# Kernel optimization log

Measured on AMD Instinct MI355X. Metric: run time of the kernel, lower is better.

Reference implementation:

```python
import jax, jax.numpy as jnp
import numpy as np

B, N, M = 8, 2048, 2048
DQ = DK = DV = H = O = 1024

def setup_inputs() -> dict:
    key = jax.random.key(0)
    ks = jax.random.split(key, 10)
    input_query = jax.random.normal(ks[0], (B, N, DQ), dtype=jnp.float32)
    input_key = jax.random.normal(ks[1], (B, M, DK), dtype=jnp.float32)
    input_value = jax.random.normal(ks[2], (B, M, DV), dtype=jnp.float32)
    seq_lens = jax.random.randint(ks[3], (B,), 1, M + 1)
    seq_lens = seq_lens.at[0].set(M)  # original asserts max(seq_lens) == M
    s = 1.0 / np.sqrt(DQ)
    Wq = jax.random.normal(ks[4], (DQ, H), dtype=jnp.float32) * s
    bq = jnp.zeros((H,), dtype=jnp.float32)
    Wk = jax.random.normal(ks[5], (DK, H), dtype=jnp.float32) * s
    bk = jnp.zeros((H,), dtype=jnp.float32)
    Wv = jax.random.normal(ks[6], (DV, O), dtype=jnp.float32) * s
    bv = jnp.zeros((O,), dtype=jnp.float32)
    return {"input_query": input_query, "input_key": input_key, "input_value": input_value,
            "seq_lens": seq_lens, "Wq": Wq, "bq": bq, "Wk": Wk, "bk": bk, "Wv": Wv, "bv": bv}


def reference(input_query, input_key, input_value, seq_lens, Wq, bq, Wk, bk, Wv, bv):
    hidden_dim = Wq.shape[1]
    lq = input_query @ Wq + bq          # (B, N, H)
    lk = input_key @ Wk + bk            # (B, M, H)
    lv = input_value @ Wv + bv          # (B, M, O)
    scores = jnp.einsum('bnh,bmh->bnm', lq, lk) / jnp.sqrt(jnp.float32(hidden_dim))
    # additive mask: 0 for valid positions, finfo.min for padded (as in original)
    valid = (jnp.arange(scores.shape[-1]) < seq_lens[:, None])[:, None, :]  # (B,1,M)
    add_mask = jnp.where(valid, 0.0, jnp.finfo(scores.dtype).min)
    scores = scores + add_mask
    probs = jax.nn.softmax(scores, axis=-1)
    out = jnp.einsum('bnm,bmo->bno', probs, lv)  # dropout is identity in eval
    return out
```

## Files before the change

kernel.cpp:

```cpp
#include <hip/hip_runtime.h>
#include <hip/hip_bf16.h>

typedef unsigned short u16;
typedef __attribute__((ext_vector_type(8))) short bfrag;
typedef __attribute__((ext_vector_type(4))) float f32x4;
typedef __attribute__((ext_vector_type(8))) unsigned short us8;
typedef __attribute__((ext_vector_type(4))) unsigned short us4;

__device__ __forceinline__ u16 f2bf(float f) {
  union { float f; unsigned int u; } x; x.f = f;
  unsigned int r = x.u + 0x7fffu + ((x.u >> 16) & 1u);
  return (u16)(r >> 16);
}
__device__ __forceinline__ float bf2f(u16 u) {
  union { unsigned int u; float f; } x; x.u = ((unsigned int)u) << 16;
  return x.f;
}

__device__ __forceinline__ void gld16(const void* g, void* l) {
  __builtin_amdgcn_global_load_lds((const __attribute__((address_space(1))) void*)g,
                                   (__attribute__((address_space(3))) void*)l, 16, 0, 0);
}

__global__ __launch_bounds__(256) void transpose_w(const float* __restrict__ W0,
                                                   const float* __restrict__ W1,
                                                   const float* __restrict__ W2,
                                                   u16* __restrict__ T0,
                                                   u16* __restrict__ T1,
                                                   u16* __restrict__ T2) {
  const float* W = (blockIdx.z == 0) ? W0 : ((blockIdx.z == 1) ? W1 : W2);
  u16* T = (blockIdx.z == 0) ? T0 : ((blockIdx.z == 1) ? T1 : T2);
  __shared__ u16 tile[64][72];
  const int t = threadIdx.x;
  const int rr = t >> 4;
  const int cc = (t & 15) * 4;
  const int kbase = blockIdx.y * 64, nbase = blockIdx.x * 64;
#pragma unroll
  for (int j = 0; j < 4; ++j) {
    int kl = rr + j * 16;
    float4 v = *(const float4*)(W + (size_t)(kbase + kl) * 1024 + nbase + cc);
    tile[kl][cc + 0] = f2bf(v.x);
    tile[kl][cc + 1] = f2bf(v.y);
    tile[kl][cc + 2] = f2bf(v.z);
    tile[kl][cc + 3] = f2bf(v.w);
  }
  __syncthreads();
#pragma unroll
  for (int j = 0; j < 4; ++j) {
    int nl = rr + j * 16;
    us4 o;
    o[0] = tile[cc + 0][nl];
    o[1] = tile[cc + 1][nl];
    o[2] = tile[cc + 2][nl];
    o[3] = tile[cc + 3][nl];
    *(us4*)(T + (size_t)(nbase + nl) * 1024 + kbase + cc) = o;
  }
}

__global__ __launch_bounds__(256) void cvt_bf16(const float* __restrict__ src,
                                                u16* __restrict__ dst, int n8) {
  int i = blockIdx.x * blockDim.x + threadIdx.x;
  const int stride = gridDim.x * blockDim.x;
  for (; i < n8; i += stride) {
    const float4* p = (const float4*)(src + (size_t)i * 8);
    float4 v0 = p[0], v1 = p[1];
    us8 o;
    o[0] = f2bf(v0.x); o[1] = f2bf(v0.y); o[2] = f2bf(v0.z); o[3] = f2bf(v0.w);
    o[4] = f2bf(v1.x); o[5] = f2bf(v1.y); o[6] = f2bf(v1.z); o[7] = f2bf(v1.w);
    *(us8*)(dst + (size_t)i * 8) = o;
  }
}

template <int OUT>
__global__ __launch_bounds__(512, 2) void gemm256(const u16* __restrict__ gA,
                                                  const u16* __restrict__ gB,
                                                  const float* __restrict__ bias,
                                                  void* __restrict__ outp,
                                                  int K, int ldc,
                                                  size_t aStride, size_t bStride,
                                                  size_t cStride,
                                                  const int* __restrict__ seq) {
  __shared__ u16 lds[65536];
  const int tid = threadIdx.x;

  const int id = blockIdx.x + gridDim.x * (blockIdx.y + gridDim.y * blockIdx.z);
  int bx, by, bz;
  if constexpr (OUT == 0 || OUT == 2) {
    bx = (id >> 3) & 3; by = (id & 7) + 8 * (id >> 5); bz = 0;
  } else if constexpr (OUT == 1) {
    bx = (id >> 3) & 7; by = id & 7; bz = id >> 6;
  } else {
    bx = (id >> 3) & 3; by = id & 7; bz = id >> 5;
  }

  const u16* A = gA + (size_t)bz * aStride;
  const u16* B = gB + (size_t)bz * bStride;
  const int brow = by * 256, bcol = bx * 256;

  const int NT = K >> 6;
  int NTe = NT;
  if constexpr (OUT == 1) {
    if (bcol >= seq[bz]) return;
  }
  if constexpr (OUT == 3) {
    const int len = seq[bz];
    const int nt2 = (len + 63) >> 6;
    NTe = nt2 < NT ? nt2 : NT;
  }

  const int wv = tid >> 6, l = tid & 63;
  const int wm = wv >> 2, wn = wv & 3;
  const int fr = l & 15, fq = l >> 4;
  const int g0 = (fq ^ (fr & 7)) * 8;
  const int g1 = ((4 + fq) ^ (fr & 7)) * 8;

  const int srow = tid >> 3;
  const int sg = (tid & 7) ^ (srow & 7);
  const u16* aS = A + (size_t)(brow + srow) * K + sg * 8;
  const u16* bS = B + (size_t)(bcol + srow) * K + sg * 8;
  u16* const dA = lds + wv * 512;
  u16* const dB = lds + 32768 + wv * 512;

  f32x4 acc[8][4] = {};

  auto stA = [&](int tile, int c, int buf) {
    gld16(aS + (size_t)tile * 64 + (size_t)c * 64 * K, dA + buf * 16384 + c * 4096);
  };
  auto stB = [&](int tile, int c, int buf) {
    gld16(bS + (size_t)tile * 64 + (size_t)c * 64 * K, dB + buf * 16384 + c * 4096);
  };

#pragma unroll
  for (int c = 0; c < 4; ++c) stA(0, c, 0);
#pragma unroll
  for (int c = 0; c < 4; ++c) stB(0, c, 0);
  if (NTe > 1) {
    stA(1, 0, 1); stA(1, 2, 1);
    stB(1, 0, 1); stB(1, 1, 1); stB(1, 2, 1); stB(1, 3, 1);
  }

  for (int t = 0; t < NTe; ++t) {
    const int cur = t & 1;
    const u16* At = lds + cur * 16384;
    const u16* Bt = lds + 32768 + cur * 16384;

    if (t + 1 < NTe) asm volatile("s_waitcnt vmcnt(6)" ::: "memory");
    else             asm volatile("s_waitcnt vmcnt(0)" ::: "memory");
    __builtin_amdgcn_s_barrier();

    bfrag a[4][2], b[2][2][2];

#pragma unroll
    for (int m = 0; m < 4; ++m) {
      const u16* p = At + (wm * 128 + m * 16 + fr) * 64;
      a[m][0] = *(const bfrag*)(p + g0);
      a[m][1] = *(const bfrag*)(p + g1);
    }
#pragma unroll
    for (int n = 0; n < 2; ++n) {
      const u16* p = Bt + (wn * 64 + n * 16 + fr) * 64;
      b[0][n][0] = *(const bfrag*)(p + g0);
      b[0][n][1] = *(const bfrag*)(p + g1);
    }
    if (t + 1 < NTe) { stA(t + 1, 1, cur ^ 1); stA(t + 1, 3, cur ^ 1); }
    __builtin_amdgcn_s_barrier();
    asm volatile("s_waitcnt lgkmcnt(0)" ::: "memory");
    __builtin_amdgcn_sched_barrier(0);
    __builtin_amdgcn_s_setprio(1);
#pragma unroll
    for (int n = 0; n < 2; ++n)
#pragma unroll
      for (int m = 0; m < 4; ++m) {
        acc[m][n] = __builtin_amdgcn_mfma_f32_16x16x32_bf16(a[m][0], b[0][n][0], acc[m][n], 0, 0, 0);
        acc[m][n] = __builtin_amdgcn_mfma_f32_16x16x32_bf16(a[m][1], b[0][n][1], acc[m][n], 0, 0, 0);
      }
    __builtin_amdgcn_s_setprio(0);
    __builtin_amdgcn_s_barrier();

#pragma unroll
    for (int n = 0; n < 2; ++n) {
      const u16* p = Bt + (wn * 64 + 32 + n * 16 + fr) * 64;
      b[1][n][0] = *(const bfrag*)(p + g0);
      b[1][n][1] = *(const bfrag*)(p + g1);
    }
    if (t + 2 < NTe) { stA(t + 2, 0, cur); stA(t + 2, 2, cur); }
    __builtin_amdgcn_s_barrier();
    asm volatile("s_waitcnt lgkmcnt(0)" ::: "memory");
    __builtin_amdgcn_sched_barrier(0);
    __builtin_amdgcn_s_setprio(1);
#pragma unroll
    for (int n = 0; n < 2; ++n)
#pragma unroll
      for (int m = 0; m < 4; ++m) {
        acc[m][2 + n] = __builtin_amdgcn_mfma_f32_16x16x32_bf16(a[m][0], b[1][n][0], acc[m][2 + n], 0, 0, 0);
        acc[m][2 + n] = __builtin_amdgcn_mfma_f32_16x16x32_bf16(a[m][1], b[1][n][1], acc[m][2 + n], 0, 0, 0);
      }
    __builtin_amdgcn_s_setprio(0);
    __builtin_amdgcn_s_barrier();

#pragma unroll
    for (int m = 0; m < 4; ++m) {
      const u16* p = At + (wm * 128 + 64 + m * 16 + fr) * 64;
      a[m][0] = *(const bfrag*)(p + g0);
      a[m][1] = *(const bfrag*)(p + g1);
    }
    if (t + 2 < NTe) { stB(t + 2, 0, cur); stB(t + 2, 1, cur); }
    __builtin_amdgcn_s_barrier();
    asm volatile("s_waitcnt lgkmcnt(0)" ::: "memory");
    __builtin_amdgcn_sched_barrier(0);
    __builtin_amdgcn_s_setprio(1);
#pragma unroll
    for (int n = 0; n < 2; ++n)
#pragma unroll
      for (int m = 0; m < 4; ++m) {
        acc[4 + m][n] = __builtin_amdgcn_mfma_f32_16x16x32_bf16(a[m][0], b[0][n][0], acc[4 + m][n], 0, 0, 0);
        acc[4 + m][n] = __builtin_amdgcn_mfma_f32_16x16x32_bf16(a[m][1], b[0][n][1], acc[4 + m][n], 0, 0, 0);
      }
    __builtin_amdgcn_s_setprio(0);
    __builtin_amdgcn_s_barrier();

    if (t + 2 < NTe) { stB(t + 2, 2, cur); stB(t + 2, 3, cur); }
    __builtin_amdgcn_s_setprio(1);
#pragma unroll
    for (int n = 0; n < 2; ++n)
#pragma unroll
      for (int m = 0; m < 4; ++m) {
        acc[4 + m][2 + n] = __builtin_amdgcn_mfma_f32_16x16x32_bf16(a[m][0], b[1][n][0], acc[4 + m][2 + n], 0, 0, 0);
        acc[4 + m][2 + n] = __builtin_amdgcn_mfma_f32_16x16x32_bf16(a[m][1], b[1][n][1], acc[4 + m][2 + n], 0, 0, 0);
      }
    __builtin_amdgcn_s_setprio(0);
  }

#pragma unroll
  for (int mg = 0; mg < 8; ++mg) {
    const int r0 = brow + wm * 128 + mg * 16 + fq * 4;
#pragma unroll
    for (int n = 0; n < 4; ++n) {
      const int c = bcol + wn * 64 + n * 16 + fr;
      f32x4 vv = acc[mg][n];
      if constexpr (OUT == 0) {
        float bb = bias[c];
        u16* C = (u16*)outp;
#pragma unroll
        for (int j = 0; j < 4; ++j) C[(size_t)(r0 + j) * ldc + c] = f2bf(vv[j] + bb);
      } else if constexpr (OUT == 1) {
        u16* C = (u16*)outp + (size_t)bz * cStride;
#pragma unroll
        for (int j = 0; j < 4; ++j) C[(size_t)(r0 + j) * ldc + c] = f2bf(vv[j] * 0.03125f);
      } else if constexpr (OUT == 2) {
        float bb = bias[c];
        const int bz2 = r0 >> 11, mm = r0 & 2047;
        us4 o;
#pragma unroll
        for (int j = 0; j < 4; ++j) o[j] = f2bf(vv[j] + bb);
        *(us4*)((u16*)outp + ((size_t)bz2 * 1024 + c) * 2048 + mm) = o;
      } else {
        float* C = (float*)outp + (size_t)bz * cStride;
#pragma unroll
        for (int j = 0; j < 4; ++j) C[(size_t)(r0 + j) * ldc + c] = vv[j];
      }
    }
  }
}

__global__ __launch_bounds__(256) void softmax_mask(u16* __restrict__ probs,
                                                    const int* __restrict__ seq) {
  const int bid = blockIdx.x;
  const int b = bid >> 11, n = bid & 2047;
  const int len = seq[b];
  const int len64 = (len + 63) & ~63;
  u16* row = probs + ((size_t)b * 2048 + n) * 2048;
  const int t = threadIdx.x;
  const int w = t >> 6, l = t & 63;

  us8 sv = {};
  if (t * 8 < len) sv = *(const us8*)(row + t * 8);
  float vals[8];
  float vmax = -1e30f;
#pragma unroll
  for (int e = 0; e < 8; ++e) {
    int m = t * 8 + e;
    float x = bf2f(sv[e]);
    vals[e] = (m < len) ? x : -1e30f;
    vmax = fmaxf(vmax, vals[e]);
  }
#pragma unroll
  for (int o = 32; o > 0; o >>= 1) vmax = fmaxf(vmax, __shfl_xor(vmax, o, 64));
  __shared__ float sm[4], ss[4];
  if (l == 0) sm[w] = vmax;
  __syncthreads();
  vmax = fmaxf(fmaxf(sm[0], sm[1]), fmaxf(sm[2], sm[3]));

  float ev[8];
  float sum = 0.f;
#pragma unroll
  for (int e = 0; e < 8; ++e) {
    int m = t * 8 + e;
    float p = (m < len) ? __expf(vals[e] - vmax) : 0.f;
    ev[e] = p;
    sum += p;
  }
#pragma unroll
  for (int o = 32; o > 0; o >>= 1) sum += __shfl_xor(sum, o, 64);
  if (l == 0) ss[w] = sum;
  __syncthreads();
  sum = ss[0] + ss[1] + ss[2] + ss[3];
  float inv = 1.f / sum;
  if (t * 8 < len64) {
    us8 ov;
#pragma unroll
    for (int e = 0; e < 8; ++e) ov[e] = f2bf(ev[e] * inv);
    *(us8*)(row + t * 8) = ov;
  }
}

extern "C" void kernel_launch(void* const* d_in, const int* in_sizes, int n_in,
                              void* d_out, int out_size, void* d_ws, size_t ws_size,
                              hipStream_t stream) {
  const float* q   = (const float*)d_in[0];
  const float* k   = (const float*)d_in[1];
  const float* v   = (const float*)d_in[2];
  const int*   seq = (const int*)d_in[3];
  const float* Wq  = (const float*)d_in[4];
  const float* bq  = (const float*)d_in[5];
  const float* Wk  = (const float*)d_in[6];
  const float* bk  = (const float*)d_in[7];
  const float* Wv  = (const float*)d_in[8];
  const float* bv  = (const float*)d_in[9];
  float* out = (float*)d_out;

  u16* ws = (u16*)d_ws;
  u16* wtq = ws;
  u16* wtk = wtq + (size_t)1024 * 1024;
  u16* wtv = wtk + (size_t)1024 * 1024;
  u16* lq  = wtv + (size_t)1024 * 1024;
  u16* lk  = lq + (size_t)16384 * 1024;
  u16* lvt = lk + (size_t)16384 * 1024;
  u16* probs = lvt + (size_t)16384 * 1024;
  u16* cbuf = probs;

  const size_t S21 = (size_t)2048 * 1024;
  const size_t S22 = (size_t)2048 * 2048;

  transpose_w<<<dim3(16, 16, 3), 256, 0, stream>>>(Wq, Wk, Wv, wtq, wtk, wtv);

  cvt_bf16<<<dim3(2048), 256, 0, stream>>>(q, cbuf, 2097152);
  gemm256<0><<<dim3(4, 64, 1), 512, 0, stream>>>(cbuf, wtq, bq, lq, 1024, 1024, 0, 0, 0, nullptr);
  cvt_bf16<<<dim3(2048), 256, 0, stream>>>(k, cbuf, 2097152);
  gemm256<0><<<dim3(4, 64, 1), 512, 0, stream>>>(cbuf, wtk, bk, lk, 1024, 1024, 0, 0, 0, nullptr);
  cvt_bf16<<<dim3(2048), 256, 0, stream>>>(v, cbuf, 2097152);
  gemm256<2><<<dim3(4, 64, 1), 512, 0, stream>>>(cbuf, wtv, bv, lvt, 1024, 1024, 0, 0, 0, nullptr);

  gemm256<1><<<dim3(8, 8, 8), 512, 0, stream>>>(lq, lk, nullptr, probs, 1024, 2048, S21, S21, S22, seq);
  softmax_mask<<<dim3(16384), 256, 0, stream>>>(probs, seq);
  gemm256<3><<<dim3(4, 8, 8), 512, 0, stream>>>(probs, lvt, nullptr, out, 2048, 1024, S22, S21, S21, seq);
}
```

Baseline: 320.8 us.

## Replace 256-tile pipelined GEMM with simpler 128-tile GEMM fusing fp32-to-bf16 conversion

Replaces the hand-pipelined 256x256 double-buffered GEMM with a simpler 128x128 single-buffered GEMM using K-step 32 and 256 threads. The projection GEMMs now read fp32 activations directly and convert them to bf16 while storing into LDS, which removes the three separate cvt_bf16 kernels and their intermediate buffer traffic. The block-id swizzle for L2 locality is also changed. The cost is losing the overlap of global loads with MFMA work, since each K step now waits on a barrier before computing, and the smaller tiles give less data reuse.

Result: slower. 397.9 us (+24.0%).

```diff
diff --git a/kernel.cpp b/kernel.cpp
--- a/kernel.cpp
+++ b/kernel.cpp
@@ -57,22 +57,8 @@
   }
 }
 
-__global__ __launch_bounds__(256) void cvt_bf16(const float* __restrict__ src,
-                                                u16* __restrict__ dst, int n8) {
-  int i = blockIdx.x * blockDim.x + threadIdx.x;
-  const int stride = gridDim.x * blockDim.x;
-  for (; i < n8; i += stride) {
-    const float4* p = (const float4*)(src + (size_t)i * 8);
-    float4 v0 = p[0], v1 = p[1];
-    us8 o;
-    o[0] = f2bf(v0.x); o[1] = f2bf(v0.y); o[2] = f2bf(v0.z); o[3] = f2bf(v0.w);
-    o[4] = f2bf(v1.x); o[5] = f2bf(v1.y); o[6] = f2bf(v1.z); o[7] = f2bf(v1.w);
-    *(us8*)(dst + (size_t)i * 8) = o;
-  }
-}
-
 template <int OUT>
-__global__ __launch_bounds__(512, 2) void gemm256(const u16* __restrict__ gA,
+__global__ __launch_bounds__(256, 4) void gemm128(const void* __restrict__ gAv,
                                                   const u16* __restrict__ gB,
                                                   const float* __restrict__ bias,
                                                   void* __restrict__ outp,
@@ -80,164 +66,105 @@
                                                   size_t aStride, size_t bStride,
                                                   size_t cStride,
                                                   const int* __restrict__ seq) {
-  __shared__ u16 lds[65536];
+  constexpr bool AF32 = (OUT == 0 || OUT == 2);
+  __shared__ u16 Ab[4096];
+  __shared__ u16 Bb[4096];
   const int tid = threadIdx.x;
 
-  const int id = blockIdx.x + gridDim.x * (blockIdx.y + gridDim.y * blockIdx.z);
   int bx, by, bz;
-  if constexpr (OUT == 0 || OUT == 2) {
-    bx = (id >> 3) & 3; by = (id & 7) + 8 * (id >> 5); bz = 0;
-  } else if constexpr (OUT == 1) {
-    bx = (id >> 3) & 7; by = id & 7; bz = id >> 6;
+  if constexpr (AF32) {
+    const int gx = gridDim.x, gy = gridDim.y;
+    const int nwg = gx * gy;
+    int id = blockIdx.x + gx * blockIdx.y;
+    id = (id & 7) * (nwg >> 3) + (id >> 3);
+    bx = id % gx; by = id / gx; bz = 0;
   } else {
-    bx = (id >> 3) & 3; by = id & 7; bz = id >> 5;
-  }
-
-  const u16* A = gA + (size_t)bz * aStride;
+    bx = blockIdx.x; by = blockIdx.y; bz = blockIdx.z;
+  }
+
   const u16* B = gB + (size_t)bz * bStride;
-  const int brow = by * 256, bcol = bx * 256;
-
-  const int NT = K >> 6;
+  const int brow = by * 128, bcol = bx * 128;
+
+  const int NT = K >> 5;
   int NTe = NT;
   if constexpr (OUT == 1) {
     if (bcol >= seq[bz]) return;
   }
   if constexpr (OUT == 3) {
     const int len = seq[bz];
-    const int nt2 = (len + 63) >> 6;
+    const int nt2 = (len + 31) >> 5;
     NTe = nt2 < NT ? nt2 : NT;
   }
 
   const int wv = tid >> 6, l = tid & 63;
-  const int wm = wv >> 2, wn = wv & 3;
+  const int wm = wv >> 1, wn = wv & 1;
   const int fr = l & 15, fq = l >> 4;
-  const int g0 = (fq ^ (fr & 7)) * 8;
-  const int g1 = ((4 + fq) ^ (fr & 7)) * 8;
-
-  const int srow = tid >> 3;
-  const int sg = (tid & 7) ^ (srow & 7);
-  const u16* aS = A + (size_t)(brow + srow) * K + sg * 8;
-  const u16* bS = B + (size_t)(bcol + srow) * K + sg * 8;
-  u16* const dA = lds + wv * 512;
-  u16* const dB = lds + 32768 + wv * 512;
-
-  f32x4 acc[8][4] = {};
-
-  auto stA = [&](int tile, int c, int buf) {
-    gld16(aS + (size_t)tile * 64 + (size_t)c * 64 * K, dA + buf * 16384 + c * 4096);
-  };
-  auto stB = [&](int tile, int c, int buf) {
-    gld16(bS + (size_t)tile * 64 + (size_t)c * 64 * K, dB + buf * 16384 + c * 4096);
-  };
-
-#pragma unroll
-  for (int c = 0; c < 4; ++c) stA(0, c, 0);
-#pragma unroll
-  for (int c = 0; c < 4; ++c) stB(0, c, 0);
-  if (NTe > 1) {
-    stA(1, 0, 1); stA(1, 2, 1);
-    stB(1, 0, 1); stB(1, 1, 1); stB(1, 2, 1); stB(1, 3, 1);
-  }
+  const int goff = (fq ^ ((fr >> 1) & 3)) * 8;
+
+  const int sr = tid >> 2;
+  const int sg = (tid & 3) ^ ((tid >> 3) & 3);
+  const int phys8 = (tid & 3) * 8;
+
+  const float* Af = (const float*)gAv;
+  const u16* Ab16 = (const u16*)gAv + (size_t)bz * aStride;
+  const u16* bS = B + (size_t)(bcol + sr) * K + sg * 8;
+  u16* const dA = Ab + wv * 512;
+  u16* const dB = Bb + wv * 512;
+
+  f32x4 acc[4][4] = {};
 
   for (int t = 0; t < NTe; ++t) {
-    const int cur = t & 1;
-    const u16* At = lds + cur * 16384;
-    const u16* Bt = lds + 32768 + cur * 16384;
-
-    if (t + 1 < NTe) asm volatile("s_waitcnt vmcnt(6)" ::: "memory");
-    else             asm volatile("s_waitcnt vmcnt(0)" ::: "memory");
-    __builtin_amdgcn_s_barrier();
-
-    bfrag a[4][2], b[2][2][2];
-
-#pragma unroll
-    for (int m = 0; m < 4; ++m) {
-      const u16* p = At + (wm * 128 + m * 16 + fr) * 64;
-      a[m][0] = *(const bfrag*)(p + g0);
-      a[m][1] = *(const bfrag*)(p + g1);
+    const int k0 = t << 5;
+    if constexpr (AF32) {
+      float4 va[2][2];
+#pragma unroll
+      for (int u = 0; u < 2; ++u) {
+        const float* ap = Af + (size_t)(brow + u * 64 + sr) * K + k0 + sg * 8;
+        va[u][0] = *(const float4*)ap;
+        va[u][1] = *(const float4*)(ap + 4);
+      }
+      gld16(bS + k0, dB);
+      gld16(bS + k0 + (size_t)64 * K, dB + 2048);
+#pragma unroll
+      for (int u = 0; u < 2; ++u) {
+        us8 pk;
+        pk[0] = f2bf(va[u][0].x); pk[1] = f2bf(va[u][0].y);
+        pk[2] = f2bf(va[u][0].z); pk[3] = f2bf(va[u][0].w);
+        pk[4] = f2bf(va[u][1].x); pk[5] = f2bf(va[u][1].y);
+        pk[6] = f2bf(va[u][1].z); pk[7] = f2bf(va[u][1].w);
+        *(us8*)(Ab + (u * 64 + sr) * 32 + phys8) = pk;
+      }
+    } else {
+      const u16* aS = Ab16 + (size_t)(brow + sr) * K + k0 + sg * 8;
+      gld16(aS, dA);
+      gld16(aS + (size_t)64 * K, dA + 2048);
+      gld16(bS + k0, dB);
+      gld16(bS + k0 + (size_t)64 * K, dB + 2048);
     }
-#pragma unroll
-    for (int n = 0; n < 2; ++n) {
-      const u16* p = Bt + (wn * 64 + n * 16 + fr) * 64;
-      b[0][n][0] = *(const bfrag*)(p + g0);
-      b[0][n][1] = *(const bfrag*)(p + g1);
-    }
-    if (t + 1 < NTe) { stA(t + 1, 1, cur ^ 1); stA(t + 1, 3, cur ^ 1); }
-    __builtin_amdgcn_s_barrier();
-    asm volatile("s_waitcnt lgkmcnt(0)" ::: "memory");
-    __builtin_amdgcn_sched_barrier(0);
-    __builtin_amdgcn_s_setprio(1);
-#pragma unroll
-    for (int n = 0; n < 2; ++n)
-#pragma unroll
-      for (int m = 0; m < 4; ++m) {
-        acc[m][n] = __builtin_amdgcn_mfma_f32_16x16x32_bf16(a[m][0], b[0][n][0], acc[m][n], 0, 0, 0);
-        acc[m][n] = __builtin_amdgcn_mfma_f32_16x16x32_bf16(a[m][1], b[0][n][1], acc[m][n], 0, 0, 0);
-      }
-    __builtin_amdgcn_s_setprio(0);
-    __builtin_amdgcn_s_barrier();
-
-#pragma unroll
-    for (int n = 0; n < 2; ++n) {
-      const u16* p = Bt + (wn * 64 + 32 + n * 16 + fr) * 64;
-      b[1][n][0] = *(const bfrag*)(p + g0);
-      b[1][n][1] = *(const bfrag*)(p + g1);
-    }
-    if (t + 2 < NTe) { stA(t + 2, 0, cur); stA(t + 2, 2, cur); }
-    __builtin_amdgcn_s_barrier();
-    asm volatile("s_waitcnt lgkmcnt(0)" ::: "memory");
-    __builtin_amdgcn_sched_barrier(0);
-    __builtin_amdgcn_s_setprio(1);
-#pragma unroll
-    for (int n = 0; n < 2; ++n)
-#pragma unroll
-      for (int m = 0; m < 4; ++m) {
-        acc[m][2 + n] = __builtin_amdgcn_mfma_f32_16x16x32_bf16(a[m][0], b[1][n][0], acc[m][2 + n], 0, 0, 0);
-        acc[m][2 + n] = __builtin_amdgcn_mfma_f32_16x16x32_bf16(a[m][1], b[1][n][1], acc[m][2 + n], 0, 0, 0);
-      }
-    __builtin_amdgcn_s_setprio(0);
-    __builtin_amdgcn_s_barrier();
-
-#pragma unroll
-    for (int m = 0; m < 4; ++m) {
-      const u16* p = At + (wm * 128 + 64 + m * 16 + fr) * 64;
-      a[m][0] = *(const bfrag*)(p + g0);
-      a[m][1] = *(const bfrag*)(p + g1);
-    }
-    if (t + 2 < NTe) { stB(t + 2, 0, cur); stB(t + 2, 1, cur); }
-    __builtin_amdgcn_s_barrier();
-    asm volatile("s_waitcnt lgkmcnt(0)" ::: "memory");
-    __builtin_amdgcn_sched_barrier(0);
-    __builtin_amdgcn_s_setprio(1);
-#pragma unroll
-    for (int n = 0; n < 2; ++n)
-#pragma unroll
-      for (int m = 0; m < 4; ++m) {
-        acc[4 + m][n] = __builtin_amdgcn_mfma_f32_16x16x32_bf16(a[m][0], b[0][n][0], acc[4 + m][n], 0, 0, 0);
-        acc[4 + m][n] = __builtin_amdgcn_mfma_f32_16x16x32_bf16(a[m][1], b[0][n][1], acc[4 + m][n], 0, 0, 0);
-      }
-    __builtin_amdgcn_s_setprio(0);
-    __builtin_amdgcn_s_barrier();
-
-    if (t + 2 < NTe) { stB(t + 2, 2, cur); stB(t + 2, 3, cur); }
-    __builtin_amdgcn_s_setprio(1);
-#pragma unroll
-    for (int n = 0; n < 2; ++n)
-#pragma unroll
-      for (int m = 0; m < 4; ++m) {
-        acc[4 + m][2 + n] = __builtin_amdgcn_mfma_f32_16x16x32_bf16(a[m][0], b[1][n][0], acc[4 + m][2 + n], 0, 0, 0);
-        acc[4 + m][2 + n] = __builtin_amdgcn_mfma_f32_16x16x32_bf16(a[m][1], b[1][n][1], acc[4 + m][2 + n], 0, 0, 0);
-      }
-    __builtin_amdgcn_s_setprio(0);
-  }
-
-#pragma unroll
-  for (int mg = 0; mg < 8; ++mg) {
-    const int r0 = brow + wm * 128 + mg * 16 + fq * 4;
+    __syncthreads();
+
+    bfrag a[4], b[4];
+#pragma unroll
+    for (int m = 0; m < 4; ++m)
+      a[m] = *(const bfrag*)(Ab + (wm * 64 + m * 16 + fr) * 32 + goff);
+#pragma unroll
+    for (int n = 0; n < 4; ++n)
+      b[n] = *(const bfrag*)(Bb + (wn * 64 + n * 16 + fr) * 32 + goff);
+#pragma unroll
+    for (int m = 0; m < 4; ++m)
+#pragma unroll
+      for (int n = 0; n < 4; ++n)
+        acc[m][n] = __builtin_amdgcn_mfma_f32_16x16x32_bf16(a[m], b[n], acc[m][n], 0, 0, 0);
+    __syncthreads();
+  }
+
+#pragma unroll
+  for (int m = 0; m < 4; ++m) {
+    const int r0 = brow + wm * 64 + m * 16 + fq * 4;
 #pragma unroll
     for (int n = 0; n < 4; ++n) {
       const int c = bcol + wn * 64 + n * 16 + fr;
-      f32x4 vv = acc[mg][n];
+      f32x4 vv = acc[m][n];
       if constexpr (OUT == 0) {
         float bb = bias[c];
         u16* C = (u16*)outp;
@@ -337,21 +264,17 @@
   u16* lk  = lq + (size_t)16384 * 1024;
   u16* lvt = lk + (size_t)16384 * 1024;
   u16* probs = lvt + (size_t)16384 * 1024;
-  u16* cbuf = probs;
 
   const size_t S21 = (size_t)2048 * 1024;
   const size_t S22 = (size_t)2048 * 2048;
 
   transpose_w<<<dim3(16, 16, 3), 256, 0, stream>>>(Wq, Wk, Wv, wtq, wtk, wtv);
 
-  cvt_bf16<<<dim3(2048), 256, 0, stream>>>(q, cbuf, 2097152);
-  gemm256<0><<<dim3(4, 64, 1), 512, 0, stream>>>(cbuf, wtq, bq, lq, 1024, 1024, 0, 0, 0, nullptr);
-  cvt_bf16<<<dim3(2048), 256, 0, stream>>>(k, cbuf, 2097152);
-  gemm256<0><<<dim3(4, 64, 1), 512, 0, stream>>>(cbuf, wtk, bk, lk, 1024, 1024, 0, 0, 0, nullptr);
-  cvt_bf16<<<dim3(2048), 256, 0, stream>>>(v, cbuf, 2097152);
-  gemm256<2><<<dim3(4, 64, 1), 512, 0, stream>>>(cbuf, wtv, bv, lvt, 1024, 1024, 0, 0, 0, nullptr);
-
-  gemm256<1><<<dim3(8, 8, 8), 512, 0, stream>>>(lq, lk, nullptr, probs, 1024, 2048, S21, S21, S22, seq);
+  gemm128<0><<<dim3(8, 128), 256, 0, stream>>>(q, wtq, bq, lq, 1024, 1024, 0, 0, 0, nullptr);
+  gemm128<0><<<dim3(8, 128), 256, 0, stream>>>(k, wtk, bk, lk, 1024, 1024, 0, 0, 0, nullptr);
+  gemm128<2><<<dim3(8, 128), 256, 0, stream>>>(v, wtv, bv, lvt, 1024, 1024, 0, 0, 0, nullptr);
+
+  gemm128<1><<<dim3(16, 16, 8), 256, 0, stream>>>(lq, lk, nullptr, probs, 1024, 2048, S21, S21, S22, seq);
   softmax_mask<<<dim3(16384), 256, 0, stream>>>(probs, seq);
-  gemm256<3><<<dim3(4, 8, 8), 512, 0, stream>>>(probs, lvt, nullptr, out, 2048, 1024, S22, S21, S21, seq);
-}
+  gemm128<3><<<dim3(8, 16, 8), 256, 0, stream>>>(probs, lvt, nullptr, out, 2048, 1024, S22, S21, S21, seq);
+}
```
